# Optimization experiments

Hardware: AMD Instinct MI355X
Metric: run time of the kernel (lower is better)

## Reference

```python
import jax
jax.config.update("jax_enable_x64", True)
import jax.numpy as jnp
import numpy as np
import math

B, L = 4, 4096
VOCAB, CVOCAB = 32000, 25000
HIDDEN, EDIM, NHEADS = 1024, 64, 8
NGRAMS = (2, 3)
TABLE_HINT = 100003
KSIZE, DILATION = 4, 3  # dilation = max ngram order
EPS = 1e-6


def _next_prime(n):
    if n <= 2:
        return 2
    c = n if n % 2 else n + 1
    while True:
        if all(c % i for i in range(3, int(math.isqrt(c)) + 1, 2)):
            return c
        c += 2


def _table_sizes():
    sizes, cur = [], TABLE_HINT
    for _ in range(NHEADS):
        p = _next_prime(cur)
        sizes.append(p)
        cur = p + 2
    return sizes


def setup_inputs():
    key = jax.random.key(0)
    ks = jax.random.split(key, 12)
    sizes = _table_sizes()  # identical for both ngram orders (same hint)
    max_s = max(sizes)
    n_orders = NGRAMS[1] - NGRAMS[0] + 1  # 2
    table_sizes = jnp.asarray(np.tile(np.array(sizes, dtype=np.int64), (n_orders, 1)))  # [2,8]
    tables = 0.01 * jax.random.normal(ks[0], (n_orders, NHEADS, max_s, EDIM), dtype=jnp.float32)
    return {
        "hidden_states": jax.random.normal(ks[1], (B, L, HIDDEN), dtype=jnp.float32),
        "token_ids": jax.random.randint(ks[2], (B, L), 0, VOCAB, dtype=jnp.int64),
        "projection": jax.random.randint(ks[3], (VOCAB,), 0, CVOCAB, dtype=jnp.int64),
        "mults2": jax.random.randint(ks[4], (NHEADS, 2), 1, 2**31 - 1, dtype=jnp.int64),
        "mults3": jax.random.randint(ks[5], (NHEADS, 3), 1, 2**31 - 1, dtype=jnp.int64),
        "table_sizes": table_sizes,
        "tables": tables,
        "w_k": (jax.random.normal(ks[6], (HIDDEN, n_orders * NHEADS * EDIM), dtype=jnp.float32) / math.sqrt(n_orders * NHEADS * EDIM)),
        "w_v": (jax.random.normal(ks[7], (HIDDEN, n_orders * NHEADS * EDIM), dtype=jnp.float32) / math.sqrt(n_orders * NHEADS * EDIM)),
        "q_norm_w": jnp.ones((HIDDEN,), dtype=jnp.float32),
        "k_norm_w": jnp.ones((HIDDEN,), dtype=jnp.float32),
        "conv_norm_w": jnp.ones((HIDDEN,), dtype=jnp.float32),
        "conv_w": 0.02 * jax.random.normal(ks[8], (HIDDEN, KSIZE), dtype=jnp.float32),
        "conv_b": jnp.zeros((HIDDEN,), dtype=jnp.float32),
    }


def _rmsnorm(x, w):
    norm = jax.lax.rsqrt(jnp.mean(jnp.square(x.astype(jnp.float32)), axis=-1, keepdims=True) + EPS)
    return (x.astype(jnp.float32) * norm).astype(x.dtype) * w


def _build_ngrams(compressed, n):
    # compressed: [B,L] int64 -> [B,L,n] causal windows with left zero pad
    p = jnp.pad(compressed, ((0, 0), (n - 1, 0)))
    return jnp.stack([p[:, i:i + compressed.shape[1]] for i in range(n)], axis=-1)


def _hash(ngrams, mults, sizes):
    # ngrams [B,L,n], mults [H,n], sizes [H] -> [B,L,H]
    prod = ngrams[:, :, None, :] * mults[None, None, :, :]  # int64
    mix = prod[..., 0]
    for i in range(1, prod.shape[-1]):
        mix = mix ^ prod[..., i]
    return jnp.abs(mix) % sizes[None, None, :]


def reference(hidden_states, token_ids, projection, mults2, mults3, table_sizes,
              tables, w_k, w_v, q_norm_w, k_norm_w, conv_norm_w, conv_w, conv_b):
    b, l, hidden = hidden_states.shape
    # ---- retrieve ----
    compressed = projection[jnp.clip(token_ids, 0, projection.shape[0] - 1)]  # [B,L]
    idx2 = _hash(_build_ngrams(compressed, 2), mults2, table_sizes[0])  # [B,L,H]
    idx3 = _hash(_build_ngrams(compressed, 3), mults3, table_sizes[1])  # [B,L,H]
    idx = jnp.concatenate([idx2, idx3], axis=-1)  # [B,L,2H] order: ngram2 heads, ngram3 heads
    n_tab = tables.shape[0] * tables.shape[1]
    tab_flat = tables.reshape(n_tab, tables.shape[2], tables.shape[3])
    emb = tab_flat[jnp.arange(n_tab), idx]  # [B,L,2H,EDIM] gather
    memory = emb.reshape(b, l, -1)  # [B,L,total_retrieval_dim]
    # ---- fuse ----
    k = jnp.einsum('bld,hd->blh', memory, w_k)
    v = jnp.einsum('bld,hd->blh', memory, w_v)
    q_n = _rmsnorm(hidden_states, q_norm_w)
    k_n = _rmsnorm(k, k_norm_w)
    scale = 1.0 / math.sqrt(hidden)
    gate = jax.nn.sigmoid(jnp.sum(q_n * k_n, axis=-1, keepdims=True) * scale)
    v_g = gate * v
    # ---- short conv (causal depthwise, dilation=3, kernel=4) ----
    h = _rmsnorm(v_g, conv_norm_w)
    pad = (KSIZE - 1) * DILATION  # 9; right padding is sliced off by [..., :L]
    hp = jnp.pad(h, ((0, 0), (pad, 0), (0, 0)))
    y = conv_b
    for j in range(KSIZE):
        y = y + hp[:, j * DILATION: j * DILATION + l, :] * conv_w[None, None, :, j]
    return jax.nn.silu(y) + v_g


if __name__ == "__main__":
    out = reference(**setup_inputs())
    print(out.shape, out.dtype)
```

## Files before the change

### kernel.cpp

```cpp
#include <hip/hip_runtime.h>
#include <hip/hip_bf16.h>
#include <math.h>

typedef unsigned short u16;
typedef __bf16 bf16x8 __attribute__((ext_vector_type(8)));
typedef float f32x4 __attribute__((ext_vector_type(4)));
typedef unsigned short u16x4 __attribute__((ext_vector_type(4)));
typedef unsigned short u16x8 __attribute__((ext_vector_type(8)));

#define BB 4
#define LL 4096
#define MTOK (BB*LL)
#define HID 1024
#define NKV 2048
#define KDIM 1024
#define VOCABN 32000
#define EPSF 1e-6f

__device__ __forceinline__ float bf2f(u16 x) {
  unsigned u = ((unsigned)x) << 16;
  return __builtin_bit_cast(float, u);
}
__device__ __forceinline__ u16 f2bf(float f) {
  unsigned u = __builtin_bit_cast(unsigned, f);
  u += 0x7FFFu + ((u >> 16) & 1u);
  return (u16)(u >> 16);
}

__global__ __launch_bounds__(256) void k_convert_w(const float* __restrict__ wk,
                                                   const float* __restrict__ wv,
                                                   u16* __restrict__ W) {
  int i = blockIdx.x * 256 + threadIdx.x;
  const int n4 = (NKV * KDIM) / 4;
  if (i >= n4) return;
  const int half = n4 / 2;
  const f32x4* src = (i < half) ? (const f32x4*)wk : (const f32x4*)wv;
  int j = (i < half) ? i : i - half;
  f32x4 v = src[j];
  u16x4 o = { f2bf(v[0]), f2bf(v[1]), f2bf(v[2]), f2bf(v[3]) };
  *(u16x4*)&W[(size_t)i * 4] = o;
}

__global__ __launch_bounds__(256) void k_gather(
    const int* __restrict__ tok, const int* __restrict__ proj,
    const int* __restrict__ m2, const int* __restrict__ m3,
    const int* __restrict__ tsz, const float* __restrict__ tables,
    int max_s, u16* __restrict__ mem) {
  __shared__ int sidx[16][16];
  const int m0 = blockIdx.x * 16;
  const int tid = threadIdx.x;
  const int tt = tid >> 4;
  const int t = tid & 15;
  const int m = m0 + tt;
  const int l = m & (LL - 1);

  long long c0, c1 = 0, c2 = 0;
  {
    int tk = tok[m];
    tk = tk < 0 ? 0 : (tk > VOCABN - 1 ? VOCABN - 1 : tk);
    c0 = proj[tk];
  }
  if (l >= 1) {
    int tk = tok[m - 1];
    tk = tk < 0 ? 0 : (tk > VOCABN - 1 ? VOCABN - 1 : tk);
    c1 = proj[tk];
  }
  if (l >= 2) {
    int tk = tok[m - 2];
    tk = tk < 0 ? 0 : (tk > VOCABN - 1 ? VOCABN - 1 : tk);
    c2 = proj[tk];
  }
  int order = t >> 3, h = t & 7;
  long long mix;
  if (order == 0) {
    mix = (c1 * (long long)m2[h * 2 + 0]) ^ (c0 * (long long)m2[h * 2 + 1]);
  } else {
    mix = (c2 * (long long)m3[h * 3 + 0]) ^ (c1 * (long long)m3[h * 3 + 1]) ^
          (c0 * (long long)m3[h * 3 + 2]);
  }
  unsigned long long um = (unsigned long long)(mix < 0 ? -mix : mix);
  unsigned long long usz = (unsigned long long)tsz[t];
  unsigned long long qq = (unsigned long long)((double)um / (double)usz);
  long long r = (long long)(um - qq * usz);
  if (r < 0) r += (long long)usz;
  else if (r >= (long long)usz) r -= (long long)usz;
  sidx[tt][t] = (int)r;
  __syncthreads();

  const int q = t;
#pragma unroll
  for (int it = 0; it < 16; ++it) {
    int idx = sidx[tt][it];
    const f32x4* src = (const f32x4*)(tables + ((size_t)it * (size_t)max_s + (size_t)idx) * 64);
    f32x4 e = src[q];
    u16x4 o = { f2bf(e[0]), f2bf(e[1]), f2bf(e[2]), f2bf(e[3]) };
    *(u16x4*)&mem[(size_t)m * HID + it * 64 + q * 4] = o;
  }
}

#define GBK2 32
#define BUF2 32768

__device__ __forceinline__ void gload16(const void* g, void* l) {
  __builtin_amdgcn_global_load_lds((__attribute__((address_space(1))) void*)(g),
                                   (__attribute__((address_space(3))) void*)(l), 16, 0, 0);
}
__device__ __forceinline__ int swz32(int x) { return x ^ (((x >> 6) & 3) << 4); }

__global__ __launch_bounds__(512, 2) void k_gemm(const u16* __restrict__ A,
                                                 const u16* __restrict__ Bw,
                                                 u16* __restrict__ C) {
  __shared__ __align__(16) char lds[131072];
  const int d = blockIdx.x;
  const int wg = (d & 7) * 64 + (d >> 3);
  const int bm = wg >> 3, bn = wg & 7;
  const int tid = threadIdx.x;
  const int w = tid >> 6, lane = tid & 63;
  const int wm = w >> 2, wn = w & 3;
  const int lm = lane & 15, kg = lane >> 4;

  const int ca0 = w * 2, ca1 = w * 2 + 1;
  const int row0 = ca0 * 16 + (lane >> 2);
  const int row1 = ca1 * 16 + (lane >> 2);
  const int off0 = row0 * KDIM + (((lane & 3) ^ (row0 & 3)) << 3);
  const int off1 = row1 * KDIM + (((lane & 3) ^ (row1 & 3)) << 3);
  const int dstA0 = ca0 * 1024 + lane * 16;
  const int dstA1 = ca1 * 1024 + lane * 16;
  const u16* Ap = A + (size_t)bm * 256 * KDIM;
  const u16* Bp = Bw + (size_t)bn * 256 * KDIM;

  int aro[8], bro[4];
#pragma unroll
  for (int mi = 0; mi < 8; ++mi)
    aro[mi] = swz32((wm * 128 + mi * 16 + lm) * 64 + kg * 16);
#pragma unroll
  for (int ni = 0; ni < 4; ++ni)
    bro[ni] = 16384 + swz32((wn * 64 + ni * 16 + lm) * 64 + kg * 16);

  f32x4 acc[8][4];
#pragma unroll
  for (int i = 0; i < 8; ++i)
#pragma unroll
    for (int j = 0; j < 4; ++j) acc[i][j] = (f32x4){0.f, 0.f, 0.f, 0.f};

#define STGA(kt, bb)                                                       \
  {                                                                        \
    char* bbase = lds + (bb) * BUF2;                                       \
    gload16(Ap + off0 + (kt) * GBK2, bbase + dstA0);                       \
    gload16(Ap + off1 + (kt) * GBK2, bbase + dstA1);                       \
  }
#define STGB(kt, bb)                                                       \
  {                                                                        \
    char* bbase = lds + (bb) * BUF2;                                       \
    gload16(Bp + off0 + (kt) * GBK2, bbase + 16384 + dstA0);               \
    gload16(Bp + off1 + (kt) * GBK2, bbase + 16384 + dstA1);               \
  }

#define TILE(t, bb, VMS, DOSTG)                                            \
  {                                                                        \
    asm volatile("s_waitcnt vmcnt(" VMS ")" ::: "memory");                 \
    __builtin_amdgcn_s_barrier();                                          \
    const char* buf = lds + (bb) * BUF2;                                   \
    bf16x8 af0[4], bfr[4], af1[4];                                         \
    _Pragma("unroll")                                                      \
    for (int mi = 0; mi < 4; ++mi) af0[mi] = *(const bf16x8*)(buf + aro[mi]); \
    _Pragma("unroll")                                                      \
    for (int ni = 0; ni < 4; ++ni) bfr[ni] = *(const bf16x8*)(buf + bro[ni]); \
    if (DOSTG) STGA((t) + 3, ((bb) + 3) & 3);                              \
    asm volatile("s_waitcnt lgkmcnt(0)" ::: "memory");                     \
    __builtin_amdgcn_sched_barrier(0);                                     \
    __builtin_amdgcn_s_setprio(1);                                         \
    _Pragma("unroll")                                                      \
    for (int mi = 0; mi < 4; ++mi)                                         \
      _Pragma("unroll")                                                    \
      for (int ni = 0; ni < 4; ++ni)                                       \
        acc[mi][ni] = __builtin_amdgcn_mfma_f32_16x16x32_bf16(af0[mi], bfr[ni], acc[mi][ni], 0, 0, 0); \
    __builtin_amdgcn_s_setprio(0);                                         \
    __builtin_amdgcn_s_barrier();                                          \
    _Pragma("unroll")                                                      \
    for (int mi = 0; mi < 4; ++mi) af1[mi] = *(const bf16x8*)(buf + aro[4 + mi]); \
    if (DOSTG) STGB((t) + 3, ((bb) + 3) & 3);                              \
    asm volatile("s_waitcnt lgkmcnt(0)" ::: "memory");                     \
    __builtin_amdgcn_sched_barrier(0);                                     \
    __builtin_amdgcn_s_setprio(1);                                         \
    _Pragma("unroll")                                                      \
    for (int mi = 0; mi < 4; ++mi)                                         \
      _Pragma("unroll")                                                    \
      for (int ni = 0; ni < 4; ++ni)                                       \
        acc[4 + mi][ni] = __builtin_amdgcn_mfma_f32_16x16x32_bf16(af1[mi], bfr[ni], acc[4 + mi][ni], 0, 0, 0); \
    __builtin_amdgcn_s_setprio(0);                                         \
  }

  STGA(0, 0); STGB(0, 0);
  STGA(1, 1); STGB(1, 1);
  STGA(2, 2); STGB(2, 2);
#pragma unroll 1
  for (int t4 = 0; t4 < 7; ++t4) {
    const int t = t4 * 4;
    TILE(t + 0, 0, "8", 1);
    TILE(t + 1, 1, "8", 1);
    TILE(t + 2, 2, "8", 1);
    TILE(t + 3, 3, "8", 1);
  }
  TILE(28, 0, "8", 1);
  TILE(29, 1, "8", 0);
  TILE(30, 2, "4", 0);
  TILE(31, 3, "0", 0);
#undef STGA
#undef STGB
#undef TILE

  __syncthreads();
  u16* tile = (u16*)lds;
#pragma unroll
  for (int mi = 0; mi < 8; ++mi)
#pragma unroll
    for (int ni = 0; ni < 4; ++ni)
#pragma unroll
      for (int jj = 0; jj < 4; ++jj) {
        int r = wm * 128 + mi * 16 + kg * 4 + jj;
        int ccol = wn * 64 + ni * 16 + lm;
        tile[r * 256 + ccol] = f2bf(acc[mi][ni][jj]);
      }
  __syncthreads();
#pragma unroll
  for (int it = 0; it < 8; ++it) {
    int r = it * 32 + (tid >> 4);
    int cb = (tid & 15) * 32;
    *(f32x4*)((char*)C + ((size_t)(bm * 256 + r) * NKV + bn * 256) * 2 + cb) =
        *(const f32x4*)((char*)tile + r * 512 + cb);
    *(f32x4*)((char*)C + ((size_t)(bm * 256 + r) * NKV + bn * 256) * 2 + cb + 16) =
        *(const f32x4*)((char*)tile + r * 512 + cb + 16);
  }
}

#define CR 32

__global__ __launch_bounds__(256, 3) void k_gateconv(
    const float* __restrict__ hidden, const u16* __restrict__ KV,
    const float* __restrict__ qw, const float* __restrict__ kw,
    const float* __restrict__ cw, const float* __restrict__ convw,
    const float* __restrict__ convb, float* __restrict__ out) {
  __shared__ u16 ring[16][1024];
  __shared__ f32x4 cwt[1024];
  const int blk = blockIdx.x;
  const int b = blk >> 7;
  const int l0 = (blk & 127) * CR;
  const int w = threadIdx.x >> 6, ln = threadIdx.x & 63;

  {
    const f32x4* cw4 = (const f32x4*)convw;
#pragma unroll
    for (int j = 0; j < 4; ++j) {
      int i = threadIdx.x * 4 + j;
      cwt[i ^ ((i >> 3) & 7)] = cw4[i];
    }
  }

  float qk[16], cwv[16];
  f32x4 cbv[4];
#pragma unroll
  for (int seg = 0; seg < 2; ++seg) {
    int c0 = seg * 512 + ln * 8;
    f32x4 qa = *(const f32x4*)&qw[c0], qb = *(const f32x4*)&qw[c0 + 4];
    f32x4 ka = *(const f32x4*)&kw[c0], kb = *(const f32x4*)&kw[c0 + 4];
    f32x4 ca = *(const f32x4*)&cw[c0], cbx = *(const f32x4*)&cw[c0 + 4];
#pragma unroll
    for (int i = 0; i < 4; ++i) {
      qk[seg * 8 + i] = qa[i] * ka[i];
      qk[seg * 8 + 4 + i] = qb[i] * kb[i];
      cwv[seg * 8 + i] = ca[i];
      cwv[seg * 8 + 4 + i] = cbx[i];
    }
    cbv[seg * 2] = *(const f32x4*)&convb[c0];
    cbv[seg * 2 + 1] = *(const f32x4*)&convb[c0 + 4];
  }
  __syncthreads();

  const int base = l0 - 12;
  f32x4 x0, x1, x2, x3, nx0, nx1, nx2, nx3;
  u16x8 kk0, kk1, vv0, vv1, nk0, nk1, nv0, nv1;

#define LOADROW(r, X0, X1, X2, X3, K0, K1, V0, V1)                             \
  {                                                                            \
    X0 = (f32x4){0.f,0.f,0.f,0.f}; X1 = X0; X2 = X0; X3 = X0;                  \
    K0 = (u16x8){0,0,0,0,0,0,0,0}; K1 = K0; V0 = K0; V1 = K0;                  \
    if ((r) >= l0 - 9 && (r) >= 0) {                                           \
      size_t mr = (size_t)b * LL + (r);                                        \
      X0 = *(const f32x4*)&hidden[mr * HID + ln * 8];                          \
      X1 = *(const f32x4*)&hidden[mr * HID + ln * 8 + 4];                      \
      X2 = *(const f32x4*)&hidden[mr * HID + 512 + ln * 8];                    \
      X3 = *(const f32x4*)&hidden[mr * HID + 512 + ln * 8 + 4];                \
      K0 = *(const u16x8*)&KV[mr * NKV + ln * 8];                              \
      K1 = *(const u16x8*)&KV[mr * NKV + 512 + ln * 8];                        \
      V0 = *(const u16x8*)&KV[mr * NKV + HID + ln * 8];                        \
      V1 = *(const u16x8*)&KV[mr * NKV + HID + 512 + ln * 8];                  \
    }                                                                          \
  }

  LOADROW(base + w, x0, x1, x2, x3, kk0, kk1, vv0, vv1);

#pragma unroll 1
  for (int g = 0; g < 11; ++g) {
    const int r = base + g * 4 + w;
    if (g < 10) {
      LOADROW(r + 4, nx0, nx1, nx2, nx3, nk0, nk1, nv0, nv1);
    }
    float s0 = 0.f, s1 = 0.f, s2 = 0.f, s3 = 0.f;
#pragma unroll
    for (int e = 0; e < 8; ++e) {
      float xa = (e < 4) ? x0[e] : x1[e - 4];
      float xb = (e < 4) ? x2[e] : x3[e - 4];
      float ka = bf2f(kk0[e]), kb = bf2f(kk1[e]);
      float va = bf2f(vv0[e]), vb = bf2f(vv1[e]);
      s0 += xa * xa + xb * xb;
      s1 += ka * ka + kb * kb;
      s2 += xa * qk[e] * ka + xb * qk[8 + e] * kb;
      s3 += va * va + vb * vb;
    }
#pragma unroll
    for (int mm = 32; mm >= 1; mm >>= 1) {
      s0 += __shfl_xor(s0, mm, 64);
      s1 += __shfl_xor(s1, mm, 64);
      s2 += __shfl_xor(s2, mm, 64);
      s3 += __shfl_xor(s3, mm, 64);
    }
    const float inv = 0.0009765625f;
    float rq = rsqrtf(s0 * inv + EPSF);
    float rk = rsqrtf(s1 * inv + EPSF);
    float gate = 1.f / (1.f + expf(-rq * rk * s2 * 0.03125f));
    float rv = rsqrtf(gate * gate * s3 * inv + EPSF);
    float grv = gate * rv;

    u16x8 h0p, h1p;
#pragma unroll
    for (int e = 0; e < 8; ++e) {
      h0p[e] = f2bf(bf2f(vv0[e]) * grv * cwv[e]);
      h1p[e] = f2bf(bf2f(vv1[e]) * grv * cwv[8 + e]);
    }
    const int slot = r & 15;
    *(u16x8*)&ring[slot][ln * 8] = h0p;
    *(u16x8*)&ring[slot][512 + ln * 8] = h1p;
    __syncthreads();

    if (r >= l0) {
      const int s9 = (r - 9) & 15, s6 = (r - 6) & 15, s3s = (r - 3) & 15;
      size_t mr = (size_t)b * LL + r;
#pragma unroll
      for (int seg = 0; seg < 2; ++seg) {
        u16x8 a9 = *(const u16x8*)&ring[s9][seg * 512 + ln * 8];
        u16x8 a6 = *(const u16x8*)&ring[s6][seg * 512 + ln * 8];
        u16x8 a3 = *(const u16x8*)&ring[s3s][seg * 512 + ln * 8];
        const u16x8 vv = seg ? vv1 : vv0;
        f32x4 ra, rb;
#pragma unroll
        for (int e = 0; e < 8; ++e) {
          const int idx = seg * 8 + e;
          float vf = bf2f(vv[e]);
          float hown = vf * grv * cwv[idx];
          int wi = seg * 512 + ln * 8 + e;
          f32x4 wv = cwt[wi ^ ((wi >> 3) & 7)];
          float y = cbv[seg * 2 + (e >> 2)][e & 3] + bf2f(a9[e]) * wv[0] +
                    bf2f(a6[e]) * wv[1] + bf2f(a3[e]) * wv[2] + hown * wv[3];
          float res = y / (1.f + expf(-y)) + gate * vf;
          if (e < 4) ra[e] = res; else rb[e - 4] = res;
        }
        *(f32x4*)&out[mr * HID + seg * 512 + ln * 8] = ra;
        *(f32x4*)&out[mr * HID + seg * 512 + ln * 8 + 4] = rb;
      }
    }
    __syncthreads();
    x0 = nx0; x1 = nx1; x2 = nx2; x3 = nx3;
    kk0 = nk0; kk1 = nk1; vv0 = nv0; vv1 = nv1;
  }
#undef LOADROW
}

extern "C" void kernel_launch(void* const* d_in, const int* in_sizes, int n_in,
                              void* d_out, int out_size, void* d_ws, size_t ws_size,
                              hipStream_t stream) {
  const float* hidden   = (const float*)d_in[0];
  const int*   tok      = (const int*)d_in[1];
  const int*   proj     = (const int*)d_in[2];
  const int*   m2       = (const int*)d_in[3];
  const int*   m3       = (const int*)d_in[4];
  const int*   tsz      = (const int*)d_in[5];
  const float* tables   = (const float*)d_in[6];
  const float* wk       = (const float*)d_in[7];
  const float* wv       = (const float*)d_in[8];
  const float* qw       = (const float*)d_in[9];
  const float* kw       = (const float*)d_in[10];
  const float* cnw      = (const float*)d_in[11];
  const float* convw    = (const float*)d_in[12];
  const float* convb    = (const float*)d_in[13];
  float* out = (float*)d_out;

  const int max_s = in_sizes[6] / (2 * 8 * 64);

  char* ws = (char*)d_ws;
  u16* mem = (u16*)ws;
  u16* W   = (u16*)(ws + (size_t)33554432);
  u16* KV  = (u16*)(ws + (size_t)33554432 + 4194304);

  k_convert_w<<<dim3((NKV * KDIM / 4 + 255) / 256), dim3(256), 0, stream>>>(wk, wv, W);
  k_gather<<<dim3(MTOK / 16), dim3(256), 0, stream>>>(tok, proj, m2, m3, tsz, tables, max_s, mem);
  k_gemm<<<dim3((MTOK / 256) * (NKV / 256)), dim3(512), 0, stream>>>(mem, W, KV);
  k_gateconv<<<dim3(BB * (LL / CR)), dim3(256), 0, stream>>>(hidden, KV, qw, kw, cnw, convw, convb, out);
}
```

Baseline: 161.6 us.

## Fuse weight conversion into gather, restructure GEMM LDS waits, drop gateconv barrier

Merges the weight fp32-to-bf16 conversion into the gather kernel as extra blocks, removing one kernel launch. In the GEMM tile loop, the second half's A-fragment loads and B staging are issued before the first MFMA batch, using a partial lgkmcnt wait, and the mid-tile barrier is removed. In gateconv, the ring buffer grows to 32 slots so the trailing per-row __syncthreads can be dropped. Conv weights move from swizzled LDS into 16 per-thread registers, with occupancy lowered to 2 blocks. These trade register pressure and occupancy for fewer barriers and launches, and removing barriers risks LDS hazards if the ring-depth reasoning is wrong.

```diff
diff --git a/kernel.cpp b/kernel.cpp
--- a/kernel.cpp
+++ b/kernel.cpp
@@ -27,28 +27,28 @@
   return (u16)(u >> 16);
 }
 
-__global__ __launch_bounds__(256) void k_convert_w(const float* __restrict__ wk,
-                                                   const float* __restrict__ wv,
-                                                   u16* __restrict__ W) {
-  int i = blockIdx.x * 256 + threadIdx.x;
-  const int n4 = (NKV * KDIM) / 4;
-  if (i >= n4) return;
-  const int half = n4 / 2;
-  const f32x4* src = (i < half) ? (const f32x4*)wk : (const f32x4*)wv;
-  int j = (i < half) ? i : i - half;
-  f32x4 v = src[j];
-  u16x4 o = { f2bf(v[0]), f2bf(v[1]), f2bf(v[2]), f2bf(v[3]) };
-  *(u16x4*)&W[(size_t)i * 4] = o;
-}
-
-__global__ __launch_bounds__(256) void k_gather(
+__global__ __launch_bounds__(256) void k_gather_conv(
     const int* __restrict__ tok, const int* __restrict__ proj,
     const int* __restrict__ m2, const int* __restrict__ m3,
     const int* __restrict__ tsz, const float* __restrict__ tables,
-    int max_s, u16* __restrict__ mem) {
+    int max_s, u16* __restrict__ mem,
+    const float* __restrict__ wk, const float* __restrict__ wv,
+    u16* __restrict__ W) {
+  const int blk = blockIdx.x;
+  const int tid = threadIdx.x;
+  if (blk >= MTOK / 16) {
+    int i = (blk - MTOK / 16) * 256 + tid;
+    const int n4 = (NKV * KDIM) / 4;
+    const int half = n4 / 2;
+    const f32x4* src = (i < half) ? (const f32x4*)wk : (const f32x4*)wv;
+    int j = (i < half) ? i : i - half;
+    f32x4 v = src[j];
+    u16x4 o = { f2bf(v[0]), f2bf(v[1]), f2bf(v[2]), f2bf(v[3]) };
+    *(u16x4*)&W[(size_t)i * 4] = o;
+    return;
+  }
   __shared__ int sidx[16][16];
-  const int m0 = blockIdx.x * 16;
-  const int tid = threadIdx.x;
+  const int m0 = blk * 16;
   const int tt = tid >> 4;
   const int t = tid & 15;
   const int m = m0 + tt;
@@ -167,7 +167,11 @@
     _Pragma("unroll")                                                      \
     for (int ni = 0; ni < 4; ++ni) bfr[ni] = *(const bf16x8*)(buf + bro[ni]); \
     if (DOSTG) STGA((t) + 3, ((bb) + 3) & 3);                              \
-    asm volatile("s_waitcnt lgkmcnt(0)" ::: "memory");                     \
+    _Pragma("unroll")                                                      \
+    for (int mi = 0; mi < 4; ++mi) af1[mi] = *(const bf16x8*)(buf + aro[4 + mi]); \
+    if (DOSTG) STGB((t) + 3, ((bb) + 3) & 3);                              \
+    __builtin_amdgcn_sched_barrier(0);                                     \
+    asm volatile("s_waitcnt lgkmcnt(4)" ::: "memory");                     \
     __builtin_amdgcn_sched_barrier(0);                                     \
     __builtin_amdgcn_s_setprio(1);                                         \
     _Pragma("unroll")                                                      \
@@ -176,10 +180,7 @@
       for (int ni = 0; ni < 4; ++ni)                                       \
         acc[mi][ni] = __builtin_amdgcn_mfma_f32_16x16x32_bf16(af0[mi], bfr[ni], acc[mi][ni], 0, 0, 0); \
     __builtin_amdgcn_s_setprio(0);                                         \
-    __builtin_amdgcn_s_barrier();                                          \
-    _Pragma("unroll")                                                      \
-    for (int mi = 0; mi < 4; ++mi) af1[mi] = *(const bf16x8*)(buf + aro[4 + mi]); \
-    if (DOSTG) STGB((t) + 3, ((bb) + 3) & 3);                              \
+    __builtin_amdgcn_sched_barrier(0);                                     \
     asm volatile("s_waitcnt lgkmcnt(0)" ::: "memory");                     \
     __builtin_amdgcn_sched_barrier(0);                                     \
     __builtin_amdgcn_s_setprio(1);                                         \
@@ -236,28 +237,19 @@
 
 #define CR 32
 
-__global__ __launch_bounds__(256, 3) void k_gateconv(
+__global__ __launch_bounds__(256, 2) void k_gateconv(
     const float* __restrict__ hidden, const u16* __restrict__ KV,
     const float* __restrict__ qw, const float* __restrict__ kw,
     const float* __restrict__ cw, const float* __restrict__ convw,
     const float* __restrict__ convb, float* __restrict__ out) {
-  __shared__ u16 ring[16][1024];
-  __shared__ f32x4 cwt[1024];
+  __shared__ u16 ring[32][1024];
   const int blk = blockIdx.x;
   const int b = blk >> 7;
   const int l0 = (blk & 127) * CR;
   const int w = threadIdx.x >> 6, ln = threadIdx.x & 63;
 
-  {
-    const f32x4* cw4 = (const f32x4*)convw;
-#pragma unroll
-    for (int j = 0; j < 4; ++j) {
-      int i = threadIdx.x * 4 + j;
-      cwt[i ^ ((i >> 3) & 7)] = cw4[i];
-    }
-  }
-
   float qk[16], cwv[16];
+  f32x4 wt[16];
   f32x4 cbv[4];
 #pragma unroll
   for (int seg = 0; seg < 2; ++seg) {
@@ -274,8 +266,9 @@
     }
     cbv[seg * 2] = *(const f32x4*)&convb[c0];
     cbv[seg * 2 + 1] = *(const f32x4*)&convb[c0 + 4];
-  }
-  __syncthreads();
+#pragma unroll
+    for (int e = 0; e < 8; ++e) wt[seg * 8 + e] = *(const f32x4*)&convw[(c0 + e) * 4];
+  }
 
   const int base = l0 - 12;
   f32x4 x0, x1, x2, x3, nx0, nx1, nx2, nx3;
@@ -338,13 +331,13 @@
       h0p[e] = f2bf(bf2f(vv0[e]) * grv * cwv[e]);
       h1p[e] = f2bf(bf2f(vv1[e]) * grv * cwv[8 + e]);
     }
-    const int slot = r & 15;
+    const int slot = r & 31;
     *(u16x8*)&ring[slot][ln * 8] = h0p;
     *(u16x8*)&ring[slot][512 + ln * 8] = h1p;
     __syncthreads();
 
     if (r >= l0) {
-      const int s9 = (r - 9) & 15, s6 = (r - 6) & 15, s3s = (r - 3) & 15;
+      const int s9 = (r - 9) & 31, s6 = (r - 6) & 31, s3s = (r - 3) & 31;
       size_t mr = (size_t)b * LL + r;
 #pragma unroll
       for (int seg = 0; seg < 2; ++seg) {
@@ -358,8 +351,7 @@
           const int idx = seg * 8 + e;
           float vf = bf2f(vv[e]);
           float hown = vf * grv * cwv[idx];
-          int wi = seg * 512 + ln * 8 + e;
-          f32x4 wv = cwt[wi ^ ((wi >> 3) & 7)];
+          f32x4 wv = wt[idx];
           float y = cbv[seg * 2 + (e >> 2)][e & 3] + bf2f(a9[e]) * wv[0] +
                     bf2f(a6[e]) * wv[1] + bf2f(a3[e]) * wv[2] + hown * wv[3];
           float res = y / (1.f + expf(-y)) + gate * vf;
@@ -369,7 +361,6 @@
         *(f32x4*)&out[mr * HID + seg * 512 + ln * 8 + 4] = rb;
       }
     }
-    __syncthreads();
     x0 = nx0; x1 = nx1; x2 = nx2; x3 = nx3;
     kk0 = nk0; kk1 = nk1; vv0 = nv0; vv1 = nv1;
   }
@@ -402,8 +393,8 @@
   u16* W   = (u16*)(ws + (size_t)33554432);
   u16* KV  = (u16*)(ws + (size_t)33554432 + 4194304);
 
-  k_convert_w<<<dim3((NKV * KDIM / 4 + 255) / 256), dim3(256), 0, stream>>>(wk, wv, W);
-  k_gather<<<dim3(MTOK / 16), dim3(256), 0, stream>>>(tok, proj, m2, m3, tsz, tables, max_s, mem);
+  k_gather_conv<<<dim3(MTOK / 16 + (NKV * KDIM / 4) / 256), dim3(256), 0, stream>>>(
+      tok, proj, m2, m3, tsz, tables, max_s, mem, wk, wv, W);
   k_gemm<<<dim3((MTOK / 256) * (NKV / 256)), dim3(512), 0, stream>>>(mem, W, KV);
   k_gateconv<<<dim3(BB * (LL / CR)), dim3(256), 0, stream>>>(hidden, KV, qw, kw, cnw, convw, convb, out);
 }
```

Result: faster. 146.4 us (median of 2 runs) (-9.4%).
